# Kernel optimization log

Measured on AMD Instinct MI355X. Metric: run time of the kernel, lower is better.

## Reference

```python
import jax, jax.numpy as jnp
import numpy as np

EMBED = 1024
HEADS = 16
HEAD_DIM = EMBED // HEADS


def setup_inputs() -> dict:
    key = jax.random.key(0)
    ks = jax.random.split(key, 11)
    B, S = 4, 2048
    scale = 1.0 / np.sqrt(EMBED)
    inp = {
        "query": jax.random.normal(ks[0], (B, S, EMBED), dtype=jnp.float32),
        "key": jax.random.normal(ks[1], (B, S, EMBED), dtype=jnp.float32),
        "value": jax.random.normal(ks[2], (B, S, EMBED), dtype=jnp.float32),
        "Wq": jax.random.normal(ks[3], (EMBED, EMBED), dtype=jnp.float32) * scale,
        "bq": jnp.zeros((EMBED,), dtype=jnp.float32),
        "Wk": jax.random.normal(ks[4], (EMBED, EMBED), dtype=jnp.float32) * scale,
        "bk": jnp.zeros((EMBED,), dtype=jnp.float32),
        "Wv": jax.random.normal(ks[5], (EMBED, EMBED), dtype=jnp.float32) * scale,
        "bv": jnp.zeros((EMBED,), dtype=jnp.float32),
        "Wo": jax.random.normal(ks[6], (EMBED, EMBED), dtype=jnp.float32) * scale,
        "bo": jnp.zeros((EMBED,), dtype=jnp.float32),
    }
    return inp


def _split_heads(x):
    # [B,S,E] -> [B,H,S,D]
    B, S, _ = x.shape
    return x.reshape(B, S, HEADS, HEAD_DIM).transpose(0, 2, 1, 3)


def reference(query, key, value, Wq, bq, Wk, bk, Wv, bv, Wo, bo):
    B, S, _ = query.shape
    q = _split_heads(query @ Wq.T + bq)   # [B,H,S,D]
    k = _split_heads(key @ Wk.T + bk)
    v = _split_heads(value @ Wv.T + bv)
    scores = jnp.einsum("bhqd,bhkd->bhqk", q, k) / jnp.sqrt(jnp.float32(HEAD_DIM))
    attn = jax.nn.softmax(scores, axis=-1)
    out = jnp.einsum("bhqk,bhkd->bhqd", attn, v)  # [B,H,S,D]
    out = out.transpose(0, 2, 1, 3).reshape(B, S, EMBED)
    return out @ Wo.T + bo
```

## Files before the change

### kernel.cpp

```cpp
#include <hip/hip_runtime.h>

typedef _Float16 f16;
typedef __attribute__((ext_vector_type(2))) __fp16 fp16x2_raw;
typedef __attribute__((ext_vector_type(4))) _Float16 f16x4;
typedef __attribute__((ext_vector_type(8))) _Float16 f16x8;
typedef __attribute__((ext_vector_type(4))) float f32x4;
typedef __attribute__((ext_vector_type(16))) float f32x16;
typedef __attribute__((ext_vector_type(2))) unsigned int u32x2;
typedef __attribute__((ext_vector_type(4))) unsigned int u32x4;

#define NB 4
#define NS 2048
#define NE 1024
#define NH 16
#define ND 64
#define NM (NB*NS)

__device__ __forceinline__ void gld16(const void* g, void* l) {
  __builtin_amdgcn_global_load_lds((const __attribute__((address_space(1))) unsigned int*)g,
                                   (__attribute__((address_space(3))) unsigned int*)l, 16, 0, 0);
}

__device__ __forceinline__ unsigned cvt2h(float a, float b) {
  fp16x2_raw r = __builtin_amdgcn_cvt_pkrtz(a, b);
  return __builtin_bit_cast(unsigned, r);
}

__device__ __forceinline__ void plswap(unsigned& a, unsigned& b) {
  asm volatile("v_permlane32_swap_b32 %0, %1" : "+v"(a), "+v"(b));
}

template<bool AF32, bool BF32, bool OUTF32>
__device__ __forceinline__
void gemm_body(const void* __restrict__ Asrc, const void* __restrict__ Bsrc,
               const float* __restrict__ bias, float* __restrict__ Cf,
               f16* __restrict__ Ch, int M, int N, int K, int id,
               f16* As, f16* Bs)
{
  const int t = threadIdx.x;
  const int l = t & 63, w = t >> 6;
  const int wr = w >> 1, wc = w & 1;

  const int xcd = id & 7, slot = id >> 3;
  const int m0 = (((slot >> 3) << 3) | xcd) * 128;
  const int n0 = (slot & 7) * 128;

  f32x4 acc[4][4];
  #pragma unroll
  for (int i = 0; i < 4; ++i)
    #pragma unroll
    for (int j = 0; j < 4; ++j)
      acc[i][j] = f32x4{0.f, 0.f, 0.f, 0.f};

  const int off0 = (w*2+0)*1024 + l*16;
  const int off1 = (w*2+1)*1024 + l*16;
  const int row0 = off0 >> 6, k0 = (off0 & 63) >> 1;
  const int row1 = off1 >> 6, k1 = (off1 & 63) >> 1;
  const f16*   a0h = (const f16*)Asrc   + (size_t)(m0+row0)*K + k0;
  const f16*   a1h = (const f16*)Asrc   + (size_t)(m0+row1)*K + k1;
  const float* a0f = (const float*)Asrc + (size_t)(m0+row0)*K + k0;
  const float* a1f = (const float*)Asrc + (size_t)(m0+row1)*K + k1;
  const float* b0f = (const float*)Bsrc + (size_t)(n0+row0)*K + k0;
  const float* b1f = (const float*)Bsrc + (size_t)(n0+row1)*K + k1;

  const int aoff = (wr*64 + (l&15))*32 + ((l>>4)<<3);
  const int boff = (wc*64 + (l&15))*32 + ((l>>4)<<3);

  {
    float4 x0 = *(const float4*)(b0f);
    float4 x1 = *(const float4*)(b0f + 4);
    float4 y0 = *(const float4*)(b1f);
    float4 y1 = *(const float4*)(b1f + 4);
    u32x4 wa, wb;
    wa[0] = cvt2h(x0.x, x0.y); wa[1] = cvt2h(x0.z, x0.w);
    wa[2] = cvt2h(x1.x, x1.y); wa[3] = cvt2h(x1.z, x1.w);
    wb[0] = cvt2h(y0.x, y0.y); wb[1] = cvt2h(y0.z, y0.w);
    wb[2] = cvt2h(y1.x, y1.y); wb[3] = cvt2h(y1.z, y1.w);
    *(u32x4*)(Bs + off0/2) = wa;
    *(u32x4*)(Bs + off1/2) = wb;
  }
  if constexpr (AF32) {
    float4 x0 = *(const float4*)(a0f);
    float4 x1 = *(const float4*)(a0f + 4);
    float4 y0 = *(const float4*)(a1f);
    float4 y1 = *(const float4*)(a1f + 4);
    u32x4 wa, wb;
    wa[0] = cvt2h(x0.x, x0.y); wa[1] = cvt2h(x0.z, x0.w);
    wa[2] = cvt2h(x1.x, x1.y); wa[3] = cvt2h(x1.z, x1.w);
    wb[0] = cvt2h(y0.x, y0.y); wb[1] = cvt2h(y0.z, y0.w);
    wb[2] = cvt2h(y1.x, y1.y); wb[3] = cvt2h(y1.z, y1.w);
    *(u32x4*)(As + off0/2) = wa;
    *(u32x4*)(As + off1/2) = wb;
  } else {
    gld16(a0h, As + off0/2);
    gld16(a1h, As + off1/2);
  }
  asm volatile("s_waitcnt vmcnt(0)" ::: "memory");
  __syncthreads();

  const int NK = K / 32;
  for (int ksi = 0; ksi < NK; ++ksi) {
    const int cur = ksi & 1, nxt = cur ^ 1;
    float4 ax0, ax1, ay0, ay1;
    float4 bx0, bx1, by0, by1;
    if (ksi < NK-1) {
      const int kt = (ksi+1) * 32;
      bx0 = *(const float4*)(b0f + kt);
      bx1 = *(const float4*)(b0f + kt + 4);
      by0 = *(const float4*)(b1f + kt);
      by1 = *(const float4*)(b1f + kt + 4);
      if constexpr (AF32) {
        ax0 = *(const float4*)(a0f + kt);
        ax1 = *(const float4*)(a0f + kt + 4);
        ay0 = *(const float4*)(a1f + kt);
        ay1 = *(const float4*)(a1f + kt + 4);
      } else {
        gld16(a0h + kt, As + nxt*4096 + off0/2);
        gld16(a1h + kt, As + nxt*4096 + off1/2);
      }
    }
    const f16* Ac = As + cur*4096;
    const f16* Bc = Bs + cur*4096;
    f16x8 af[4], bf[4];
    #pragma unroll
    for (int i = 0; i < 4; ++i) af[i] = *(const f16x8*)(Ac + aoff + i*512);
    #pragma unroll
    for (int j = 0; j < 4; ++j) bf[j] = *(const f16x8*)(Bc + boff + j*512);
    #pragma unroll
    for (int i = 0; i < 4; ++i)
      #pragma unroll
      for (int j = 0; j < 4; ++j)
        acc[i][j] = __builtin_amdgcn_mfma_f32_16x16x32_f16(af[i], bf[j], acc[i][j], 0, 0, 0);
    asm volatile("s_waitcnt vmcnt(0)" ::: "memory");
    if (ksi < NK-1) {
      {
        u32x4 wa, wb;
        wa[0] = cvt2h(bx0.x, bx0.y); wa[1] = cvt2h(bx0.z, bx0.w);
        wa[2] = cvt2h(bx1.x, bx1.y); wa[3] = cvt2h(bx1.z, bx1.w);
        wb[0] = cvt2h(by0.x, by0.y); wb[1] = cvt2h(by0.z, by0.w);
        wb[2] = cvt2h(by1.x, by1.y); wb[3] = cvt2h(by1.z, by1.w);
        *(u32x4*)(Bs + nxt*4096 + off0/2) = wa;
        *(u32x4*)(Bs + nxt*4096 + off1/2) = wb;
      }
      if constexpr (AF32) {
        u32x4 wa, wb;
        wa[0] = cvt2h(ax0.x, ax0.y); wa[1] = cvt2h(ax0.z, ax0.w);
        wa[2] = cvt2h(ax1.x, ax1.y); wa[3] = cvt2h(ax1.z, ax1.w);
        wb[0] = cvt2h(ay0.x, ay0.y); wb[1] = cvt2h(ay0.z, ay0.w);
        wb[2] = cvt2h(ay1.x, ay1.y); wb[3] = cvt2h(ay1.z, ay1.w);
        *(u32x4*)(As + nxt*4096 + off0/2) = wa;
        *(u32x4*)(As + nxt*4096 + off1/2) = wb;
      }
    }
    __syncthreads();
  }

  #pragma unroll
  for (int j = 0; j < 4; ++j) {
    const int col = n0 + wc*64 + j*16 + (l & 15);
    const float bb = bias[col];
    #pragma unroll
    for (int i = 0; i < 4; ++i) {
      const int rowb = m0 + wr*64 + i*16 + ((l>>4)<<2);
      #pragma unroll
      for (int r = 0; r < 4; ++r) {
        float v = acc[i][j][r] + bb;
        if constexpr (OUTF32) Cf[(size_t)(rowb+r)*N + col] = v;
        else                  Ch[(size_t)(rowb+r)*N + col] = (f16)v;
      }
    }
  }
}

__global__ __launch_bounds__(256)
void gemm_qkv(const float* __restrict__ q_in, const float* __restrict__ k_in,
              const float* __restrict__ v_in, const float* __restrict__ Wq,
              const float* __restrict__ Wk, const float* __restrict__ Wv,
              const float* __restrict__ bq, const float* __restrict__ bk,
              const float* __restrict__ bv, f16* __restrict__ Qp,
              f16* __restrict__ Kp, f16* __restrict__ Vp)
{
  __shared__ __align__(16) f16 As[2*128*32];
  __shared__ __align__(16) f16 Bs[2*128*32];
  const int z = blockIdx.z;
  const float* Asrc = (z == 0) ? q_in : (z == 1) ? k_in : v_in;
  const float* Bsrc = (z == 0) ? Wq : (z == 1) ? Wk : Wv;
  const float* bias = (z == 0) ? bq : (z == 1) ? bk : bv;
  f16* Ch = (z == 0) ? Qp : (z == 1) ? Kp : Vp;
  const int id = blockIdx.x + blockIdx.y * gridDim.x;
  gemm_body<true, true, false>(Asrc, Bsrc, bias, nullptr, Ch, NM, NE, NE, id, As, Bs);
}

__global__ __launch_bounds__(256)
void gemm_out(const f16* __restrict__ Op, const float* __restrict__ Wo,
              const float* __restrict__ bo, float* __restrict__ Out)
{
  __shared__ __align__(16) f16 As[2*128*32];
  __shared__ __align__(16) f16 Bs[2*128*32];
  const int id = blockIdx.x + blockIdx.y * gridDim.x;
  gemm_body<false, true, true>(Op, Wo, bo, Out, nullptr, NM, NE, NE, id, As, Bs);
}

__global__ __launch_bounds__(256, 4)
void attn_kernel(const f16* __restrict__ Q, const f16* __restrict__ K,
                 const f16* __restrict__ V, f16* __restrict__ O)
{
  __shared__ __align__(16) f16 S_lds[16384];

  const int t = threadIdx.x, l = t & 63, w = t >> 6;
  const int lq = l & 31, hi = l >> 5;

  const int lin = blockIdx.x + (blockIdx.y << 4);
  const int xcd = lin & 7, jj = lin >> 3;
  const int bh = xcd * 8 + (jj >> 4);
  const int qt = jj & 15;
  const int b = bh >> 4, h = bh & 15;
  const size_t base = (size_t)b * NS * NE + (size_t)h * ND;
  const int q = qt*128 + w*32 + lq;

  f16x8 bq[4];
  #pragma unroll
  for (int ks = 0; ks < 4; ++ks)
    bq[ks] = *(const f16x8*)&Q[base + (size_t)q*NE + ks*16 + hi*8];
  asm volatile("s_waitcnt vmcnt(0)" ::: "memory");

  f32x16 o[2];
  #pragma unroll
  for (int dt = 0; dt < 2; ++dt)
    #pragma unroll
    for (int r = 0; r < 16; ++r) o[dt][r] = 0.f;
  float m2 = -3e38f, lsum = 0.f;
  const float K2 = 0.125f * 1.44269504089f;

  const int krow0 = w*16 + (l>>3);
  const int kgran = ((l&7) ^ (l>>3)) * 8;
  const f16* kSrc0 = K + base + (size_t)krow0*NE + kgran;
  const f16* kSrc1 = kSrc0 + (size_t)8*NE;
  const f16* vSrc = V + base + (size_t)l*NE + w*16;

  const size_t tileAdv = (size_t)64 * NE;
  const int kd0 = (w*2+0)*512 + l*8;
  const int kd1 = (w*2+1)*512 + l*8;

  f16x8 va, vb;
  {
    gld16(kSrc0, &S_lds[0] + kd0);
    gld16(kSrc1, &S_lds[0] + kd1);
    va = *(const f16x8*)(vSrc);
    vb = *(const f16x8*)(vSrc + 8);
    asm volatile("s_waitcnt vmcnt(0)" ::: "memory");
    char* vt0 = (char*)&S_lds[4096];
    #pragma unroll
    for (int i = 0; i < 8; ++i) {
      const int d0 = w*16 + i, d1 = w*16 + 8 + i;
      *(f16*)(vt0 + ((d0*128 + l*2) ^ ((i & 7) << 4))) = va[i];
      *(f16*)(vt0 + ((d1*128 + l*2) ^ ((i & 7) << 4))) = vb[i];
    }
  }
  __syncthreads();

  for (int it = 0; it < 32; ++it) {
    const int cur = it & 1, nb = cur ^ 1;
    const char* ksb = (const char*)(&S_lds[cur*8192]);
    const char* vtb = (const char*)(&S_lds[cur*8192 + 4096]);

    if (it < 31) {
      const size_t g = (size_t)(it+1) * tileAdv;
      gld16(kSrc0 + g, &S_lds[nb*8192] + kd0);
      gld16(kSrc1 + g, &S_lds[nb*8192] + kd1);
      va = *(const f16x8*)(vSrc + g);
      vb = *(const f16x8*)(vSrc + g + 8);
    }

    f32x16 s[2];
    #pragma unroll
    for (int ct = 0; ct < 2; ++ct)
      #pragma unroll
      for (int r = 0; r < 16; ++r) s[ct][r] = 0.f;
    __builtin_amdgcn_s_setprio(1);
    #pragma unroll
    for (int ct = 0; ct < 2; ++ct) {
      const int krow = ct*32 + lq;
      const int rswz = (krow & 7) << 4;
      #pragma unroll
      for (int ks = 0; ks < 4; ++ks) {
        f16x8 ak = *(const f16x8*)(ksb + ((krow*128 + ks*32 + hi*16) ^ rswz));
        s[ct] = __builtin_amdgcn_mfma_f32_32x32x16_f16(ak, bq[ks], s[ct], 0, 0, 0);
      }
    }
    __builtin_amdgcn_s_setprio(0);

    float mm[16];
    #pragma unroll
    for (int r = 0; r < 16; ++r) mm[r] = fmaxf(s[0][r], s[1][r]);
    #pragma unroll
    for (int st = 8; st > 0; st >>= 1)
      #pragma unroll
      for (int r = 0; r < st; ++r) mm[r] = fmaxf(mm[r], mm[r+st]);
    float mx = mm[0] * K2;
    mx = fmaxf(mx, __shfl_xor(mx, 32));

    if (__any(mx > m2 + 8.0f)) {
      const float mnew = fmaxf(m2, mx);
      const float alpha = __builtin_amdgcn_exp2f(m2 - mnew);
      m2 = mnew;
      lsum *= alpha;
      #pragma unroll
      for (int dt = 0; dt < 2; ++dt)
        #pragma unroll
        for (int r = 0; r < 16; ++r) o[dt][r] *= alpha;
    }

    float ps4[4] = {0.f, 0.f, 0.f, 0.f};
    #pragma unroll
    for (int ct = 0; ct < 2; ++ct)
      #pragma unroll
      for (int r = 0; r < 16; ++r) {
        float p = __builtin_amdgcn_exp2f(s[ct][r]*K2 - m2);
        s[ct][r] = p;
        ps4[r & 3] += p;
      }
    lsum += (ps4[0] + ps4[1]) + (ps4[2] + ps4[3]);

    f16x8 pa[4];
    #pragma unroll
    for (int ct = 0; ct < 2; ++ct) {
      unsigned wd[8];
      #pragma unroll
      for (int m = 0; m < 4; ++m)
        #pragma unroll
        for (int hh = 0; hh < 2; ++hh)
          wd[m*2 + hh] = cvt2h(s[ct][4*m + 2*hh], s[ct][4*m + 2*hh + 1]);
      #pragma unroll
      for (int ks2 = 0; ks2 < 2; ++ks2) {
        unsigned a0 = wd[(2*ks2)*2 + 0], b0 = wd[(2*ks2+1)*2 + 0];
        unsigned a1 = wd[(2*ks2)*2 + 1], b1 = wd[(2*ks2+1)*2 + 1];
        plswap(a0, b0);
        plswap(a1, b1);
        union { unsigned u[4]; f16x8 v; } pp;
        pp.u[0] = a0; pp.u[1] = a1; pp.u[2] = b0; pp.u[3] = b1;
        pa[ct*2 + ks2] = pp.v;
      }
    }

    __builtin_amdgcn_s_setprio(1);
    #pragma unroll
    for (int ks = 0; ks < 4; ++ks)
      #pragma unroll
      for (int dt = 0; dt < 2; ++dt) {
        const int drow = dt*32 + lq;
        f16x8 av = *(const f16x8*)(vtb + ((drow*128 + ks*32 + hi*16) ^ ((drow & 7) << 4)));
        o[dt] = __builtin_amdgcn_mfma_f32_32x32x16_f16(av, pa[ks], o[dt], 0, 0, 0);
      }
    __builtin_amdgcn_s_setprio(0);

    if (it < 31) {
      asm volatile("s_waitcnt vmcnt(0)" ::: "memory");
      char* vtn = (char*)(&S_lds[nb*8192 + 4096]);
      #pragma unroll
      for (int i = 0; i < 8; ++i) {
        const int d0 = w*16 + i, d1 = w*16 + 8 + i;
        *(f16*)(vtn + ((d0*128 + l*2) ^ ((i & 7) << 4))) = va[i];
        *(f16*)(vtn + ((d1*128 + l*2) ^ ((i & 7) << 4))) = vb[i];
      }
      __syncthreads();
    }
  }

  const float lt = lsum + __shfl_xor(lsum, 32);
  const float linv = 1.0f / lt;
  #pragma unroll
  for (int dt = 0; dt < 2; ++dt)
    #pragma unroll
    for (int m = 0; m < 4; ++m) {
      u32x2 st;
      st.x = cvt2h(o[dt][4*m+0]*linv, o[dt][4*m+1]*linv);
      st.y = cvt2h(o[dt][4*m+2]*linv, o[dt][4*m+3]*linv);
      const int d = dt*32 + 8*m + 4*hi;
      *(u32x2*)&O[base + (size_t)q*NE + d] = st;
    }
}

extern "C" void kernel_launch(void* const* d_in, const int* in_sizes, int n_in,
                              void* d_out, int out_size, void* d_ws, size_t ws_size,
                              hipStream_t stream)
{
  const float* q_in = (const float*)d_in[0];
  const float* k_in = (const float*)d_in[1];
  const float* v_in = (const float*)d_in[2];
  const float* Wq = (const float*)d_in[3];
  const float* bq = (const float*)d_in[4];
  const float* Wk = (const float*)d_in[5];
  const float* bk = (const float*)d_in[6];
  const float* Wv = (const float*)d_in[7];
  const float* bv = (const float*)d_in[8];
  const float* Wo = (const float*)d_in[9];
  const float* bo = (const float*)d_in[10];

  char* ws = (char*)d_ws;
  f16* Qp   = (f16*)(ws + 58720256);
  f16* Kp   = (f16*)(ws + 75497472);
  f16* Vp   = (f16*)(ws + 92274688);
  f16* Op   = (f16*)(ws + 109051904);

  gemm_qkv<<<dim3(8, 64, 3), 256, 0, stream>>>(q_in, k_in, v_in, Wq, Wk, Wv,
                                               bq, bk, bv, Qp, Kp, Vp);

  attn_kernel<<<dim3(16, 64), 256, 0, stream>>>(Qp, Kp, Vp, Op);

  gemm_out<<<dim3(8, 64), 256, 0, stream>>>(Op, Wo, bo, (float*)d_out);
}
```

Measured before the change: 234.7 us.

## Deepen GEMM global prefetch to two stages with register-staged loads

Restructures the projection GEMM main loop into a 2x unrolled loop that keeps two K-tiles of global loads in flight in registers, so loads for tile k+2 are issued while tile k is computed. The f16 A path of the output GEMM switches from global_load_lds to plain register loads and LDS stores. K and N become compile-time constants. The intent is to hide global memory latency better, at the cost of more live registers, which may lower occupancy or cause spills.

```diff
diff --git a/kernel.cpp b/kernel.cpp
--- a/kernel.cpp
+++ b/kernel.cpp
@@ -30,13 +30,20 @@
   asm volatile("v_permlane32_swap_b32 %0, %1" : "+v"(a), "+v"(b));
 }
 
-template<bool AF32, bool BF32, bool OUTF32>
+__device__ __forceinline__ u32x4 pack8(float4 x0, float4 x1) {
+  u32x4 r;
+  r[0] = cvt2h(x0.x, x0.y); r[1] = cvt2h(x0.z, x0.w);
+  r[2] = cvt2h(x1.x, x1.y); r[3] = cvt2h(x1.z, x1.w);
+  return r;
+}
+
+template<bool AF32, bool OUTF32>
 __device__ __forceinline__
-void gemm_body(const void* __restrict__ Asrc, const void* __restrict__ Bsrc,
+void gemm_body(const void* __restrict__ Asrc, const float* __restrict__ Bsrc,
                const float* __restrict__ bias, float* __restrict__ Cf,
-               f16* __restrict__ Ch, int M, int N, int K, int id,
-               f16* As, f16* Bs)
+               f16* __restrict__ Ch, int id, f16* As, f16* Bs)
 {
+  const int K = NE, N = NE;
   const int t = threadIdx.x;
   const int l = t & 63, w = t >> 6;
   const int wr = w >> 1, wc = w & 1;
@@ -60,100 +67,110 @@
   const f16*   a1h = (const f16*)Asrc   + (size_t)(m0+row1)*K + k1;
   const float* a0f = (const float*)Asrc + (size_t)(m0+row0)*K + k0;
   const float* a1f = (const float*)Asrc + (size_t)(m0+row1)*K + k1;
-  const float* b0f = (const float*)Bsrc + (size_t)(n0+row0)*K + k0;
-  const float* b1f = (const float*)Bsrc + (size_t)(n0+row1)*K + k1;
+  const float* b0f = Bsrc + (size_t)(n0+row0)*K + k0;
+  const float* b1f = Bsrc + (size_t)(n0+row1)*K + k1;
 
   const int aoff = (wr*64 + (l&15))*32 + ((l>>4)<<3);
   const int boff = (wc*64 + (l&15))*32 + ((l>>4)<<3);
 
+  float4 B0x0, B0x1, B0y0, B0y1, B1x0, B1x1, B1y0, B1y1;
+  float4 A0x0, A0x1, A0y0, A0y1, A1x0, A1x1, A1y0, A1y1;
+  f16x8  H0a, H0b, H1a, H1b;
+
   {
-    float4 x0 = *(const float4*)(b0f);
-    float4 x1 = *(const float4*)(b0f + 4);
-    float4 y0 = *(const float4*)(b1f);
-    float4 y1 = *(const float4*)(b1f + 4);
-    u32x4 wa, wb;
-    wa[0] = cvt2h(x0.x, x0.y); wa[1] = cvt2h(x0.z, x0.w);
-    wa[2] = cvt2h(x1.x, x1.y); wa[3] = cvt2h(x1.z, x1.w);
-    wb[0] = cvt2h(y0.x, y0.y); wb[1] = cvt2h(y0.z, y0.w);
-    wb[2] = cvt2h(y1.x, y1.y); wb[3] = cvt2h(y1.z, y1.w);
-    *(u32x4*)(Bs + off0/2) = wa;
-    *(u32x4*)(Bs + off1/2) = wb;
+    B0x0 = *(const float4*)(b0f);     B0x1 = *(const float4*)(b0f + 4);
+    B0y0 = *(const float4*)(b1f);     B0y1 = *(const float4*)(b1f + 4);
+    *(u32x4*)(Bs + off0/2) = pack8(B0x0, B0x1);
+    *(u32x4*)(Bs + off1/2) = pack8(B0y0, B0y1);
+    if constexpr (AF32) {
+      A0x0 = *(const float4*)(a0f);   A0x1 = *(const float4*)(a0f + 4);
+      A0y0 = *(const float4*)(a1f);   A0y1 = *(const float4*)(a1f + 4);
+      *(u32x4*)(As + off0/2) = pack8(A0x0, A0x1);
+      *(u32x4*)(As + off1/2) = pack8(A0y0, A0y1);
+    } else {
+      H0a = *(const f16x8*)(a0h);     H0b = *(const f16x8*)(a1h);
+      *(f16x8*)(As + off0/2) = H0a;
+      *(f16x8*)(As + off1/2) = H0b;
+    }
+    B1x0 = *(const float4*)(b0f + 32);  B1x1 = *(const float4*)(b0f + 36);
+    B1y0 = *(const float4*)(b1f + 32);  B1y1 = *(const float4*)(b1f + 36);
+    if constexpr (AF32) {
+      A1x0 = *(const float4*)(a0f + 32);  A1x1 = *(const float4*)(a0f + 36);
+      A1y0 = *(const float4*)(a1f + 32);  A1y1 = *(const float4*)(a1f + 36);
+    } else {
+      H1a = *(const f16x8*)(a0h + 32);    H1b = *(const f16x8*)(a1h + 32);
+    }
   }
-  if constexpr (AF32) {
-    float4 x0 = *(const float4*)(a0f);
-    float4 x1 = *(const float4*)(a0f + 4);
-    float4 y0 = *(const float4*)(a1f);
-    float4 y1 = *(const float4*)(a1f + 4);
-    u32x4 wa, wb;
-    wa[0] = cvt2h(x0.x, x0.y); wa[1] = cvt2h(x0.z, x0.w);
-    wa[2] = cvt2h(x1.x, x1.y); wa[3] = cvt2h(x1.z, x1.w);
-    wb[0] = cvt2h(y0.x, y0.y); wb[1] = cvt2h(y0.z, y0.w);
-    wb[2] = cvt2h(y1.x, y1.y); wb[3] = cvt2h(y1.z, y1.w);
-    *(u32x4*)(As + off0/2) = wa;
-    *(u32x4*)(As + off1/2) = wb;
-  } else {
-    gld16(a0h, As + off0/2);
-    gld16(a1h, As + off1/2);
-  }
-  asm volatile("s_waitcnt vmcnt(0)" ::: "memory");
   __syncthreads();
 
-  const int NK = K / 32;
-  for (int ksi = 0; ksi < NK; ++ksi) {
-    const int cur = ksi & 1, nxt = cur ^ 1;
-    float4 ax0, ax1, ay0, ay1;
-    float4 bx0, bx1, by0, by1;
-    if (ksi < NK-1) {
-      const int kt = (ksi+1) * 32;
-      bx0 = *(const float4*)(b0f + kt);
-      bx1 = *(const float4*)(b0f + kt + 4);
-      by0 = *(const float4*)(b1f + kt);
-      by1 = *(const float4*)(b1f + kt + 4);
+  #define GB_COMPUTE(BUFOFF)                                                     \
+    {                                                                            \
+      const f16* Ac = As + (BUFOFF);                                             \
+      const f16* Bc = Bs + (BUFOFF);                                             \
+      f16x8 af[4], bf[4];                                                        \
+      _Pragma("unroll")                                                          \
+      for (int i = 0; i < 4; ++i) af[i] = *(const f16x8*)(Ac + aoff + i*512);    \
+      _Pragma("unroll")                                                          \
+      for (int j = 0; j < 4; ++j) bf[j] = *(const f16x8*)(Bc + boff + j*512);    \
+      _Pragma("unroll")                                                          \
+      for (int i = 0; i < 4; ++i)                                                \
+        _Pragma("unroll")                                                        \
+        for (int j = 0; j < 4; ++j)                                              \
+          acc[i][j] = __builtin_amdgcn_mfma_f32_16x16x32_f16(af[i], bf[j], acc[i][j], 0, 0, 0); \
+    }
+
+  for (int ksi = 0; ksi < 32; ksi += 2) {
+    const bool ld0 = (ksi + 2 < 32);
+    if (ld0) {
+      const int kt = (ksi + 2) * 32;
+      B0x0 = *(const float4*)(b0f + kt);  B0x1 = *(const float4*)(b0f + kt + 4);
+      B0y0 = *(const float4*)(b1f + kt);  B0y1 = *(const float4*)(b1f + kt + 4);
       if constexpr (AF32) {
-        ax0 = *(const float4*)(a0f + kt);
-        ax1 = *(const float4*)(a0f + kt + 4);
-        ay0 = *(const float4*)(a1f + kt);
-        ay1 = *(const float4*)(a1f + kt + 4);
+        A0x0 = *(const float4*)(a0f + kt);  A0x1 = *(const float4*)(a0f + kt + 4);
+        A0y0 = *(const float4*)(a1f + kt);  A0y1 = *(const float4*)(a1f + kt + 4);
       } else {
-        gld16(a0h + kt, As + nxt*4096 + off0/2);
-        gld16(a1h + kt, As + nxt*4096 + off1/2);
-      }
-    }
-    const f16* Ac = As + cur*4096;
-    const f16* Bc = Bs + cur*4096;
-    f16x8 af[4], bf[4];
-    #pragma unroll
-    for (int i = 0; i < 4; ++i) af[i] = *(const f16x8*)(Ac + aoff + i*512);
-    #pragma unroll
-    for (int j = 0; j < 4; ++j) bf[j] = *(const f16x8*)(Bc + boff + j*512);
-    #pragma unroll
-    for (int i = 0; i < 4; ++i)
-      #pragma unroll
-      for (int j = 0; j < 4; ++j)
-        acc[i][j] = __builtin_amdgcn_mfma_f32_16x16x32_f16(af[i], bf[j], acc[i][j], 0, 0, 0);
-    asm volatile("s_waitcnt vmcnt(0)" ::: "memory");
-    if (ksi < NK-1) {
-      {
-        u32x4 wa, wb;
-        wa[0] = cvt2h(bx0.x, bx0.y); wa[1] = cvt2h(bx0.z, bx0.w);
-        wa[2] = cvt2h(bx1.x, bx1.y); wa[3] = cvt2h(bx1.z, bx1.w);
-        wb[0] = cvt2h(by0.x, by0.y); wb[1] = cvt2h(by0.z, by0.w);
-        wb[2] = cvt2h(by1.x, by1.y); wb[3] = cvt2h(by1.z, by1.w);
-        *(u32x4*)(Bs + nxt*4096 + off0/2) = wa;
-        *(u32x4*)(Bs + nxt*4096 + off1/2) = wb;
-      }
+        H0a = *(const f16x8*)(a0h + kt);    H0b = *(const f16x8*)(a1h + kt);
+      }
+    }
+    GB_COMPUTE(0)
+    *(u32x4*)(Bs + 4096 + off0/2) = pack8(B1x0, B1x1);
+    *(u32x4*)(Bs + 4096 + off1/2) = pack8(B1y0, B1y1);
+    if constexpr (AF32) {
+      *(u32x4*)(As + 4096 + off0/2) = pack8(A1x0, A1x1);
+      *(u32x4*)(As + 4096 + off1/2) = pack8(A1y0, A1y1);
+    } else {
+      *(f16x8*)(As + 4096 + off0/2) = H1a;
+      *(f16x8*)(As + 4096 + off1/2) = H1b;
+    }
+    __syncthreads();
+
+    const bool ld1 = (ksi + 3 < 32);
+    if (ld1) {
+      const int kt = (ksi + 3) * 32;
+      B1x0 = *(const float4*)(b0f + kt);  B1x1 = *(const float4*)(b0f + kt + 4);
+      B1y0 = *(const float4*)(b1f + kt);  B1y1 = *(const float4*)(b1f + kt + 4);
       if constexpr (AF32) {
-        u32x4 wa, wb;
-        wa[0] = cvt2h(ax0.x, ax0.y); wa[1] = cvt2h(ax0.z, ax0.w);
-        wa[2] = cvt2h(ax1.x, ax1.y); wa[3] = cvt2h(ax1.z, ax1.w);
-        wb[0] = cvt2h(ay0.x, ay0.y); wb[1] = cvt2h(ay0.z, ay0.w);
-        wb[2] = cvt2h(ay1.x, ay1.y); wb[3] = cvt2h(ay1.z, ay1.w);
-        *(u32x4*)(As + nxt*4096 + off0/2) = wa;
-        *(u32x4*)(As + nxt*4096 + off1/2) = wb;
+        A1x0 = *(const float4*)(a0f + kt);  A1x1 = *(const float4*)(a0f + kt + 4);
+        A1y0 = *(const float4*)(a1f + kt);  A1y1 = *(const float4*)(a1f + kt + 4);
+      } else {
+        H1a = *(const f16x8*)(a0h + kt);    H1b = *(const f16x8*)(a1h + kt);
+      }
+    }
+    GB_COMPUTE(4096)
+    if (ld0) {
+      *(u32x4*)(Bs + off0/2) = pack8(B0x0, B0x1);
+      *(u32x4*)(Bs + off1/2) = pack8(B0y0, B0y1);
+      if constexpr (AF32) {
+        *(u32x4*)(As + off0/2) = pack8(A0x0, A0x1);
+        *(u32x4*)(As + off1/2) = pack8(A0y0, A0y1);
+      } else {
+        *(f16x8*)(As + off0/2) = H0a;
+        *(f16x8*)(As + off1/2) = H0b;
       }
     }
     __syncthreads();
   }
+  #undef GB_COMPUTE
 
   #pragma unroll
   for (int j = 0; j < 4; ++j) {
@@ -188,7 +205,7 @@
   const float* bias = (z == 0) ? bq : (z == 1) ? bk : bv;
   f16* Ch = (z == 0) ? Qp : (z == 1) ? Kp : Vp;
   const int id = blockIdx.x + blockIdx.y * gridDim.x;
-  gemm_body<true, true, false>(Asrc, Bsrc, bias, nullptr, Ch, NM, NE, NE, id, As, Bs);
+  gemm_body<true, false>(Asrc, Bsrc, bias, nullptr, Ch, id, As, Bs);
 }
 
 __global__ __launch_bounds__(256)
@@ -198,7 +215,7 @@
   __shared__ __align__(16) f16 As[2*128*32];
   __shared__ __align__(16) f16 Bs[2*128*32];
   const int id = blockIdx.x + blockIdx.y * gridDim.x;
-  gemm_body<false, true, true>(Op, Wo, bo, Out, nullptr, NM, NE, NE, id, As, Bs);
+  gemm_body<false, true>(Op, Wo, bo, Out, nullptr, id, As, Bs);
 }
 
 __global__ __launch_bounds__(256, 4)
```

Result: faster. 219.1 us, median of 2 (-6.7%).
